# Optimization experiments

Hardware: AMD Instinct MI355X
Metric: run time of the kernel (lower is better)

Reference implementation:

```python
import jax, jax.numpy as jnp
import numpy as np

TOPK = 8
EPS = 1e-12  # matches torch F.normalize default eps


def setup_inputs() -> dict:
    key = jax.random.key(0)
    x = jax.random.normal(key, (8, 2048, 128), dtype=jnp.float32)
    return {"x": x}


def reference(x) -> jnp.ndarray:
    B, N, D = x.shape
    # --- pairwise dot scores on L2-normalized features (cosine similarity) ---
    norm = jnp.sqrt(jnp.sum(x * x, axis=-1, keepdims=True))
    normed = x / jnp.maximum(norm, EPS)
    scores = jnp.einsum('bnd,bmd->bnm', normed, normed)  # [B, N, N]

    # --- top-k per row -> binary adjacency via scatter ---
    _, idx = jax.lax.top_k(scores, TOPK)  # [B, N, k]
    bi = jnp.arange(B)[:, None, None]
    ni = jnp.arange(N)[None, :, None]
    adj = jnp.zeros((B, N, N), dtype=x.dtype).at[bi, ni, idx].set(1.0)

    # --- symmetrize and add self loops ---
    adj = jnp.maximum(adj, jnp.swapaxes(adj, 1, 2))
    eye = jnp.eye(N, dtype=x.dtype)
    adj = jnp.maximum(adj, eye[None, :, :])
    return adj
```

## Files before the change

kernel.cpp:

```cpp
#include <hip/hip_runtime.h>
#include <cstdint>

#define NN 2048
#define DD 128
#define BATCH 8
#define NROWS 16384
#define MARGIN 0.02f
#define CAP2 64

typedef __attribute__((ext_vector_type(8))) short bf16x8;
typedef __attribute__((ext_vector_type(4))) float f32x4;
typedef unsigned long long u64;
typedef unsigned int u32;
typedef unsigned short u16;

__device__ __forceinline__ u32 bf16rne(float f) {
  u32 u = __float_as_uint(f);
  return (u + 0x7fffu + ((u >> 16) & 1u)) >> 16;
}
__device__ __forceinline__ u32 bf16up(float f) {
  const u32 u = __float_as_uint(f);
  return (u + (((int)u >= 0) ? 0xFFFFu : 0u)) >> 16;
}

__global__ __launch_bounds__(256) void k_normalize(const float* __restrict__ x,
                                                   double* __restrict__ rinv,
                                                   u32* __restrict__ nb,
                                                   float4* __restrict__ outz) {
  const int wave = threadIdx.x >> 6, lane = threadIdx.x & 63;
  const long long row = (long long)blockIdx.x * 4 + wave;
  float2 v = ((const float2*)(x + row * DD))[lane];
  const double d0 = v.x, d1 = v.y;
  double s = d0 * d0 + d1 * d1;
  #pragma unroll
  for (int m = 32; m >= 1; m >>= 1) s += __shfl_xor(s, m, 64);
  double den = sqrt(s); den = den > 1e-12 ? den : 1e-12;
  if (lane == 0) rinv[row] = 1.0 / den;
  double2 o; o.x = d0 / den; o.y = d1 / den;
  nb[row * (DD / 2) + lane] = bf16rne((float)o.x) | (bf16rne((float)o.y) << 16);

  {
    const int base = blockIdx.x * 256 + threadIdx.x;
    const float4 zf = {0.0f, 0.0f, 0.0f, 0.0f};
    #pragma unroll
    for (int k = 0; k < 8; ++k) outz[base + k * 1048576] = zf;
  }
}

#define CXF(i, j) { const float a_ = L[i], b_ = L[j]; L[i] = fmaxf(a_, b_); L[j] = fminf(a_, b_); }
__device__ __forceinline__ void merge8f(float (&kv)[8], const float (&ov)[8]) {
  float L[8];
  #pragma unroll
  for (int i = 0; i < 8; ++i) L[i] = fmaxf(kv[i], ov[7 - i]);
  CXF(0, 4) CXF(1, 5) CXF(2, 6) CXF(3, 7)
  CXF(0, 2) CXF(1, 3) CXF(4, 6) CXF(5, 7)
  CXF(0, 1) CXF(2, 3) CXF(4, 5) CXF(6, 7)
  #pragma unroll
  for (int i = 0; i < 8; ++i) kv[i] = L[i];
}

__device__ __forceinline__ u64 make_key(double s, int col) {
  u64 u = (u64)__double_as_longlong(s);
  const u64 m = (u64)((long long)u >> 63);
  u ^= (m | 0x8000000000000000ull);
  return (u & ~2047ull) | (u64)(2047 - col);
}
__device__ __forceinline__ u64 umax64(u64 a, u64 b) { return a > b ? a : b; }
__device__ __forceinline__ u64 umin64(u64 a, u64 b) { return a > b ? b : a; }
__device__ __forceinline__ void merge8(u64 (&kv)[8], const u64 (&ov)[8]) {
  u64 L[8];
  #pragma unroll
  for (int i = 0; i < 8; ++i) L[i] = umax64(kv[i], ov[7 - i]);
#define CX(i, j) { const u64 a_ = L[i], b_ = L[j]; L[i] = umax64(a_, b_); L[j] = umin64(a_, b_); }
  CX(0, 4) CX(1, 5) CX(2, 6) CX(3, 7)
  CX(0, 2) CX(1, 3) CX(4, 6) CX(5, 7)
  CX(0, 1) CX(2, 3) CX(4, 5) CX(6, 7)
#undef CX
  #pragma unroll
  for (int i = 0; i < 8; ++i) kv[i] = L[i];
}
__device__ __forceinline__ void insert8u(u64 (&v)[8], u64 nk) {
  if (nk > v[7]) {
    v[7] = nk;
    #pragma unroll
    for (int q = 7; q >= 1; --q) {
      const u64 a = v[q - 1], b = v[q];
      const bool sw = b > a;
      v[q - 1] = sw ? b : a; v[q] = sw ? a : b;
    }
  }
}

__global__ __launch_bounds__(1024, 4) void k_build(const u32* __restrict__ nb,
                                                   const float* __restrict__ x,
                                                   const double* __restrict__ rinv,
                                                   float* __restrict__ out) {
  __shared__ float bmf[32][130];
  __shared__ float thl[32];
  __shared__ u32 cnt[32];
  __shared__ u32 cand[32][CAP2];

  const int tid = threadIdx.x; const int w = tid >> 6; const int l = tid & 63;
  const int q = l >> 4; const int m = l & 15;
  const int b = blockIdx.x & 7;
  const int rowblk = blockIdx.x >> 3;
  const int row0 = b * NN + rowblk * 32;
  const long long brow = (long long)b * NN;

  bf16x8 pvals = {0,0,0,0,0,0,0,0}, pones = {0,0,0,0,0,0,0,0};
  if (q == 0) {
    pvals[0] = (short)(__float_as_uint((float)(m + 1)) >> 16);
    pones[0] = (short)(__float_as_uint(1.0f) >> 16);
  }
  const f32x4 z4 = {0.0f, 0.0f, 0.0f, 0.0f};
  const f32x4 pr  = __builtin_amdgcn_mfma_f32_16x16x32_bf16(pvals, pones, z4, 0, 0, 0);
  const f32x4 pr2 = __builtin_amdgcn_mfma_f32_16x16x32_bf16(pones, pvals, z4, 0, 0, 0);
  int cof[4];
  #pragma unroll
  for (int p = 0; p < 4; ++p) cof[p] = (int)pr[p] - 1;
  const int rof = (int)pr2[0] - 1;

  if (tid < 32) cnt[tid] = 0u;

  bf16x8 ar4[2][4];
  #pragma unroll
  for (int rf = 0; rf < 2; ++rf) {
    const u32* Ap = nb + (long long)(row0 + 16 * rf + m) * (DD / 2) + 4 * q;
    #pragma unroll
    for (int cc = 0; cc < 4; ++cc) ar4[rf][cc] = *(const bf16x8*)(Ap + 16 * cc);
  }

  const int c0w = w * 128;
  const u32* Bb = nb + (brow + c0w) * (DD / 2);
  bf16x8 bc[4];
  uint2 pk[16];

  #pragma unroll
  for (int t = 0; t < 8; ++t) {
    { const u32* p_ = Bb + (long long)(16 * t + m) * (DD / 2) + 4 * q;
      #pragma unroll
      for (int cc = 0; cc < 4; ++cc) bc[cc] = *(const bf16x8*)(p_ + 16 * cc); }
    #pragma unroll
    for (int rf = 0; rf < 2; ++rf) {
      f32x4 acc = z4;
      #pragma unroll
      for (int cc = 0; cc < 4; ++cc)
        acc = __builtin_amdgcn_mfma_f32_16x16x32_bf16(bc[cc], ar4[rf][cc], acc, 0, 0, 0);
      float bm_ = fmaxf(fmaxf(acc[0], acc[1]), fmaxf(acc[2], acc[3]));
      bm_ = fmaxf(bm_, __shfl_xor(bm_, 16, 64));
      bm_ = fmaxf(bm_, __shfl_xor(bm_, 32, 64));
      if (q == 0) bmf[16 * rf + m][w * 8 + t] = bm_;
      pk[t * 2 + rf].x = bf16up(acc[0]) | (bf16up(acc[1]) << 16);
      pk[t * 2 + rf].y = bf16up(acc[2]) | (bf16up(acc[3]) << 16);
    }
  }
  __syncthreads();

  for (int j = 0; j < 2; ++j) {
    const int rib = w * 2 + j;
    const float b0 = bmf[rib][2 * l];
    const float b1 = bmf[rib][2 * l + 1];
    float mx = fmaxf(b0, b1);
    float kv8[8];
    {
      const float o  = __shfl_xor(mx, 1, 64);
      const float h2 = fmaxf(mx, o), l2 = fminf(mx, o);
      const float p0 = __shfl_xor(h2, 2, 64), p1 = __shfl_xor(l2, 2, 64);
      const float m0 = fmaxf(h2, p0);
      const float xx = fminf(h2, p0);
      const float yy = fmaxf(l2, p1);
      const float m3 = fminf(l2, p1);
      const float m1 = fmaxf(xx, yy);
      const float m2 = fminf(xx, yy);
      const float q0 = __shfl_xor(m0, 4, 64), q1 = __shfl_xor(m1, 4, 64);
      const float q2 = __shfl_xor(m2, 4, 64), q3 = __shfl_xor(m3, 4, 64);
      float L[8] = {m0, m1, m2, m3, q3, q2, q1, q0};
      CXF(0, 4) CXF(1, 5) CXF(2, 6) CXF(3, 7)
      CXF(0, 2) CXF(1, 3) CXF(4, 6) CXF(5, 7)
      CXF(0, 1) CXF(2, 3) CXF(4, 5) CXF(6, 7)
      #pragma unroll
      for (int s = 0; s < 8; ++s) kv8[s] = L[s];
      #pragma unroll
      for (int mk = 8; mk <= 32; mk <<= 1) {
        float ov[8];
        #pragma unroll
        for (int s = 0; s < 8; ++s) ov[s] = __shfl_xor(kv8[s], mk, 64);
        merge8f(kv8, ov);
      }
    }
    if (l == 0) thl[rib] = kv8[7] - MARGIN;
  }
  __syncthreads();

  {
    float th2[2]; int rib2[2];
    #pragma unroll
    for (int rf = 0; rf < 2; ++rf) {
      rib2[rf] = 16 * rf + rof;
      th2[rf] = thl[rib2[rf]];
    }
    #pragma unroll
    for (int t = 0; t < 8; ++t)
      #pragma unroll
      for (int rf = 0; rf < 2; ++rf) {
        const uint2 pv = pk[t * 2 + rf];
        const float v0 = __uint_as_float(pv.x << 16);
        const float v1 = __uint_as_float(pv.x & 0xFFFF0000u);
        const float v2 = __uint_as_float(pv.y << 16);
        const float v3 = __uint_as_float(pv.y & 0xFFFF0000u);
        #pragma unroll
        for (int p = 0; p < 4; ++p) {
          const float vv = (p == 0) ? v0 : (p == 1) ? v1 : (p == 2) ? v2 : v3;
          if (vv >= th2[rf]) {
            const u32 id = atomicAdd(&cnt[rib2[rf]], 1u);
            if (id < CAP2) cand[rib2[rf]][id] = (u32)(c0w + 16 * t + cof[p]);
          }
        }
      }
  }
  __syncthreads();

  for (int j = 0; j < 2; ++j) {
    const int rib = w * 2 + j;
    const int r = row0 + rib;
    const int n = r & (NN - 1);
    const int c = (int)cnt[rib];
    const double ri = rinv[r];
    u64 kv[8];
    #pragma unroll
    for (int s = 0; s < 8; ++s) kv[s] = 0ull;

    if (c <= CAP2) {
      float2 a4[4];
      #pragma unroll
      for (int jj = 0; jj < 4; ++jj)
        a4[jj] = ((const float2*)(x + (long long)r * DD))[m + 16 * jj];

      for (int i = 0; i < c; i += 4) {
        const int gi = i + q;
        const bool valid = gi < c;
        const int col = valid ? (int)cand[rib][gi] : 0;
        const float2* cp = (const float2*)(x + (brow + col) * DD);
        double d = 0.0;
        #pragma unroll
        for (int jj = 0; jj < 4; ++jj) {
          const float2 bv = cp[m + 16 * jj];
          d = fma((double)a4[jj].x, (double)bv.x, d);
          d = fma((double)a4[jj].y, (double)bv.y, d);
        }
        #pragma unroll
        for (int mk = 1; mk <= 8; mk <<= 1) d += __shfl_xor(d, mk, 64);
        if (valid) insert8u(kv, make_key(d * ri * rinv[brow + col], col));
      }
      #pragma unroll
      for (int mk = 16; mk <= 32; mk <<= 1) {
        u64 ov[8];
        #pragma unroll
        for (int s = 0; s < 8; ++s) ov[s] = __shfl_xor(kv[s], mk, 64);
        merge8(kv, ov);
      }
    } else {
      for (int base = 0; base < NN; base += 64) {
        const int col = base + l;
        const float* ap = x + (long long)r * DD;
        const float* cp2 = x + (brow + col) * DD;
        double d = 0.0;
        for (int kk = 0; kk < 64; ++kk) {
          const float2 av = ((const float2*)ap)[kk];
          const float2 bv = ((const float2*)cp2)[kk];
          d = fma((double)av.x, (double)bv.x, fma((double)av.y, (double)bv.y, d));
        }
        d = d * ri * rinv[brow + col];
        u64 one[8];
        one[0] = make_key(d, col);
        #pragma unroll
        for (int s = 1; s < 8; ++s) one[s] = 0ull;
        #pragma unroll
        for (int mk = 1; mk <= 32; mk <<= 1) {
          u64 ov[8];
          #pragma unroll
          for (int s = 0; s < 8; ++s) ov[s] = __shfl_xor(one[s], mk, 64);
          merge8(one, ov);
        }
        merge8(kv, one);
      }
    }

    const long long orow = (long long)r * NN;
    const long long obase = brow * NN;
    if (l == 8) out[orow + n] = 1.0f;
    #pragma unroll
    for (int s = 0; s < 8; ++s) {
      const int mcol = 2047 - (int)(kv[s] & 2047ull);
      if (l == s) {
        out[orow + mcol] = 1.0f;
        out[obase + (long long)mcol * NN + n] = 1.0f;
      }
    }
  }
}

extern "C" void kernel_launch(void* const* d_in, const int* in_sizes, int n_in,
                              void* d_out, int out_size, void* d_ws, size_t ws_size,
                              hipStream_t stream) {
  const float* x = (const float*)d_in[0];
  float* out = (float*)d_out;
  char* ws = (char*)d_ws;
  u32* nb = (u32*)ws;
  double* rinv = (double*)(ws + 4194304);

  hipLaunchKernelGGL(k_normalize, dim3(NROWS / 4), dim3(256), 0, stream, x, rinv, nb,
                     (float4*)out);
  hipLaunchKernelGGL(k_build, dim3(512), dim3(1024), 0, stream, nb, x, rinv, out);
}
```

Before: 225.8 us.

## Split exact rescoring into separate kernel and double-buffer B tile loads

Moves the exact fp64 rescoring and output scatter out of the 1024-thread build kernel into a new 256-thread kernel with one wave per row. Candidate counts and lists pass between the two kernels through global workspace. This spreads the irregular rescoring across many more small blocks and avoids holding the large build kernel's resources during that phase. It also double-buffers the bf16 B-fragment loads in the MFMA loop, at the cost of an extra launch, a global round trip for candidates, and more registers.

```diff
diff --git a/kernel.cpp b/kernel.cpp
--- a/kernel.cpp
+++ b/kernel.cpp
@@ -92,9 +92,8 @@
 }
 
 __global__ __launch_bounds__(1024, 4) void k_build(const u32* __restrict__ nb,
-                                                   const float* __restrict__ x,
-                                                   const double* __restrict__ rinv,
-                                                   float* __restrict__ out) {
+                                                   u32* __restrict__ gcnt,
+                                                   u32* __restrict__ gcand) {
   __shared__ float bmf[32][130];
   __shared__ float thl[32];
   __shared__ u32 cnt[32];
@@ -132,28 +131,34 @@
 
   const int c0w = w * 128;
   const u32* Bb = nb + (brow + c0w) * (DD / 2);
-  bf16x8 bc[4];
+  bf16x8 bcA[4], bcB[4];
   uint2 pk[16];
 
-  #pragma unroll
-  for (int t = 0; t < 8; ++t) {
-    { const u32* p_ = Bb + (long long)(16 * t + m) * (DD / 2) + 4 * q;
-      #pragma unroll
-      for (int cc = 0; cc < 4; ++cc) bc[cc] = *(const bf16x8*)(p_ + 16 * cc); }
-    #pragma unroll
-    for (int rf = 0; rf < 2; ++rf) {
-      f32x4 acc = z4;
-      #pragma unroll
-      for (int cc = 0; cc < 4; ++cc)
-        acc = __builtin_amdgcn_mfma_f32_16x16x32_bf16(bc[cc], ar4[rf][cc], acc, 0, 0, 0);
-      float bm_ = fmaxf(fmaxf(acc[0], acc[1]), fmaxf(acc[2], acc[3]));
-      bm_ = fmaxf(bm_, __shfl_xor(bm_, 16, 64));
-      bm_ = fmaxf(bm_, __shfl_xor(bm_, 32, 64));
-      if (q == 0) bmf[16 * rf + m][w * 8 + t] = bm_;
-      pk[t * 2 + rf].x = bf16up(acc[0]) | (bf16up(acc[1]) << 16);
-      pk[t * 2 + rf].y = bf16up(acc[2]) | (bf16up(acc[3]) << 16);
-    }
-  }
+#define LOADB(DST, T) { const u32* p_ = Bb + (long long)(16 * (T) + m) * (DD / 2) + 4 * q; \
+  _Pragma("unroll") for (int cc = 0; cc < 4; ++cc) DST[cc] = *(const bf16x8*)(p_ + 16 * cc); }
+#define TILE1(BC, T) {                                                             \
+    _Pragma("unroll") for (int rf = 0; rf < 2; ++rf) {                             \
+      f32x4 acc = z4;                                                              \
+      _Pragma("unroll") for (int cc = 0; cc < 4; ++cc)                             \
+        acc = __builtin_amdgcn_mfma_f32_16x16x32_bf16(BC[cc], ar4[rf][cc], acc, 0, 0, 0); \
+      float bm_ = fmaxf(fmaxf(acc[0], acc[1]), fmaxf(acc[2], acc[3]));             \
+      bm_ = fmaxf(bm_, __shfl_xor(bm_, 16, 64));                                   \
+      bm_ = fmaxf(bm_, __shfl_xor(bm_, 32, 64));                                   \
+      if (q == 0) bmf[16 * rf + m][w * 8 + (T)] = bm_;                             \
+      pk[(T) * 2 + rf].x = bf16up(acc[0]) | (bf16up(acc[1]) << 16);                \
+      pk[(T) * 2 + rf].y = bf16up(acc[2]) | (bf16up(acc[3]) << 16);                \
+    } }
+
+  LOADB(bcA, 0)
+  #pragma unroll
+  for (int t = 0; t < 8; t += 2) {
+    LOADB(bcB, t + 1)
+    TILE1(bcA, t)
+    if (t + 2 < 8) LOADB(bcA, t + 2)
+    TILE1(bcB, t + 1)
+  }
+#undef LOADB
+#undef TILE1
   __syncthreads();
 
   for (int j = 0; j < 2; ++j) {
@@ -211,7 +216,7 @@
         #pragma unroll
         for (int p = 0; p < 4; ++p) {
           const float vv = (p == 0) ? v0 : (p == 1) ? v1 : (p == 2) ? v2 : v3;
-          if (vv >= th2[rf]) {
+          if (vv >= th2[p & 0] + 0.0f * p, vv >= th2[rf]) {
             const u32 id = atomicAdd(&cnt[rib2[rf]], 1u);
             if (id < CAP2) cand[rib2[rf]][id] = (u32)(c0w + 16 * t + cof[p]);
           }
@@ -220,82 +225,100 @@
   }
   __syncthreads();
 
-  for (int j = 0; j < 2; ++j) {
-    const int rib = w * 2 + j;
-    const int r = row0 + rib;
-    const int n = r & (NN - 1);
-    const int c = (int)cnt[rib];
-    const double ri = rinv[r];
-    u64 kv[8];
-    #pragma unroll
-    for (int s = 0; s < 8; ++s) kv[s] = 0ull;
-
-    if (c <= CAP2) {
-      float2 a4[4];
-      #pragma unroll
-      for (int jj = 0; jj < 4; ++jj)
-        a4[jj] = ((const float2*)(x + (long long)r * DD))[m + 16 * jj];
-
-      for (int i = 0; i < c; i += 4) {
-        const int gi = i + q;
-        const bool valid = gi < c;
-        const int col = valid ? (int)cand[rib][gi] : 0;
-        const float2* cp = (const float2*)(x + (brow + col) * DD);
-        double d = 0.0;
-        #pragma unroll
-        for (int jj = 0; jj < 4; ++jj) {
-          const float2 bv = cp[m + 16 * jj];
-          d = fma((double)a4[jj].x, (double)bv.x, d);
-          d = fma((double)a4[jj].y, (double)bv.y, d);
-        }
-        #pragma unroll
-        for (int mk = 1; mk <= 8; mk <<= 1) d += __shfl_xor(d, mk, 64);
-        if (valid) insert8u(kv, make_key(d * ri * rinv[brow + col], col));
-      }
-      #pragma unroll
-      for (int mk = 16; mk <= 32; mk <<= 1) {
+  {
+    const int row = tid >> 5;
+    const int sl = tid & 31;
+    if (sl == 0) gcnt[row0 + row] = cnt[row];
+    gcand[(long long)(row0 + row) * CAP2 + sl] = cand[row][sl];
+    gcand[(long long)(row0 + row) * CAP2 + sl + 32] = cand[row][sl + 32];
+  }
+}
+
+__global__ __launch_bounds__(256) void k_rescore(const u32* __restrict__ gcnt,
+                                                 const u32* __restrict__ gcand,
+                                                 const float* __restrict__ x,
+                                                 const double* __restrict__ rinv,
+                                                 float* __restrict__ out) {
+  const int w = threadIdx.x >> 6, l = threadIdx.x & 63;
+  const int q = l >> 4, m = l & 15;
+  const int b = blockIdx.x & 7;
+  const int idx = blockIdx.x >> 3;
+  const int r = b * NN + idx * 4 + w;
+  const int n = r & (NN - 1);
+  const long long brow = r - n;
+
+  const int c = (int)gcnt[r];
+  const double ri = rinv[r];
+  u64 kv[8];
+  #pragma unroll
+  for (int s = 0; s < 8; ++s) kv[s] = 0ull;
+
+  if (c <= CAP2) {
+    float2 a4[4];
+    #pragma unroll
+    for (int jj = 0; jj < 4; ++jj)
+      a4[jj] = ((const float2*)(x + (long long)r * DD))[m + 16 * jj];
+    const u32* crow = gcand + (long long)r * CAP2;
+
+    for (int i = 0; i < c; i += 4) {
+      const int gi = i + q;
+      const bool valid = gi < c;
+      const int col = valid ? (int)crow[gi] : 0;
+      const float2* cp = (const float2*)(x + (brow + col) * DD);
+      double d = 0.0;
+      #pragma unroll
+      for (int jj = 0; jj < 4; ++jj) {
+        const float2 bv = cp[m + 16 * jj];
+        d = fma((double)a4[jj].x, (double)bv.x, d);
+        d = fma((double)a4[jj].y, (double)bv.y, d);
+      }
+      #pragma unroll
+      for (int mk = 1; mk <= 8; mk <<= 1) d += __shfl_xor(d, mk, 64);
+      if (valid) insert8u(kv, make_key(d * ri * rinv[brow + col], col));
+    }
+    #pragma unroll
+    for (int mk = 16; mk <= 32; mk <<= 1) {
+      u64 ov[8];
+      #pragma unroll
+      for (int s = 0; s < 8; ++s) ov[s] = __shfl_xor(kv[s], mk, 64);
+      merge8(kv, ov);
+    }
+  } else {
+    for (int base = 0; base < NN; base += 64) {
+      const int col = base + l;
+      const float* ap = x + (long long)r * DD;
+      const float* cp2 = x + (brow + col) * DD;
+      double d = 0.0;
+      for (int kk = 0; kk < 64; ++kk) {
+        const float2 av = ((const float2*)ap)[kk];
+        const float2 bv = ((const float2*)cp2)[kk];
+        d = fma((double)av.x, (double)bv.x, fma((double)av.y, (double)bv.y, d));
+      }
+      d = d * ri * rinv[brow + col];
+      u64 one[8];
+      one[0] = make_key(d, col);
+      #pragma unroll
+      for (int s = 1; s < 8; ++s) one[s] = 0ull;
+      #pragma unroll
+      for (int mk = 1; mk <= 32; mk <<= 1) {
         u64 ov[8];
         #pragma unroll
-        for (int s = 0; s < 8; ++s) ov[s] = __shfl_xor(kv[s], mk, 64);
-        merge8(kv, ov);
-      }
-    } else {
-      for (int base = 0; base < NN; base += 64) {
-        const int col = base + l;
-        const float* ap = x + (long long)r * DD;
-        const float* cp2 = x + (brow + col) * DD;
-        double d = 0.0;
-        for (int kk = 0; kk < 64; ++kk) {
-          const float2 av = ((const float2*)ap)[kk];
-          const float2 bv = ((const float2*)cp2)[kk];
-          d = fma((double)av.x, (double)bv.x, fma((double)av.y, (double)bv.y, d));
-        }
-        d = d * ri * rinv[brow + col];
-        u64 one[8];
-        one[0] = make_key(d, col);
-        #pragma unroll
-        for (int s = 1; s < 8; ++s) one[s] = 0ull;
-        #pragma unroll
-        for (int mk = 1; mk <= 32; mk <<= 1) {
-          u64 ov[8];
-          #pragma unroll
-          for (int s = 0; s < 8; ++s) ov[s] = __shfl_xor(one[s], mk, 64);
-          merge8(one, ov);
-        }
-        merge8(kv, one);
-      }
-    }
-
-    const long long orow = (long long)r * NN;
-    const long long obase = brow * NN;
-    if (l == 8) out[orow + n] = 1.0f;
-    #pragma unroll
-    for (int s = 0; s < 8; ++s) {
-      const int mcol = 2047 - (int)(kv[s] & 2047ull);
-      if (l == s) {
-        out[orow + mcol] = 1.0f;
-        out[obase + (long long)mcol * NN + n] = 1.0f;
-      }
+        for (int s = 0; s < 8; ++s) ov[s] = __shfl_xor(one[s], mk, 64);
+        merge8(one, ov);
+      }
+      merge8(kv, one);
+    }
+  }
+
+  const long long orow = (long long)r * NN;
+  const long long obase = brow * NN;
+  if (l == 8) out[orow + n] = 1.0f;
+  #pragma unroll
+  for (int s = 0; s < 8; ++s) {
+    const int mcol = 2047 - (int)(kv[s] & 2047ull);
+    if (l == s) {
+      out[orow + mcol] = 1.0f;
+      out[obase + (long long)mcol * NN + n] = 1.0f;
     }
   }
 }
@@ -308,8 +331,12 @@
   char* ws = (char*)d_ws;
   u32* nb = (u32*)ws;
   double* rinv = (double*)(ws + 4194304);
+  u32* gcnt = (u32*)(ws + 4325376);
+  u32* gcand = (u32*)(ws + 4390912);
 
   hipLaunchKernelGGL(k_normalize, dim3(NROWS / 4), dim3(256), 0, stream, x, rinv, nb,
                      (float4*)out);
-  hipLaunchKernelGGL(k_build, dim3(512), dim3(1024), 0, stream, nb, x, rinv, out);
-}
+  hipLaunchKernelGGL(k_build, dim3(512), dim3(1024), 0, stream, nb, gcnt, gcand);
+  hipLaunchKernelGGL(k_rescore, dim3(NROWS / 4), dim3(256), 0, stream, gcnt, gcand,
+                     x, rinv, out);
+}
```

Result: slower. 233.2 us (+3.3%).
